# Kernel tuning notes

Hardware: AMD Instinct MI355X
Metric: run time of the kernel (lower is better)

The kernel has to match this reference:

```python
import jax, jax.numpy as jnp
import numpy as np

B = 524288   # samples
H = 16       # n_neuron[-1] for every node


def setup_inputs() -> dict:
    key = jax.random.key(0)
    ks = jax.random.split(key, 5)

    def w(k, shape, fan_in):
        return jax.random.normal(k, shape, jnp.float32) * (1.0 / np.sqrt(fan_in))

    return {
        "x":  jax.random.normal(ks[0], (B, 16), jnp.float32),
        # level 1: 8 nodes, each Linear(2 -> 16)
        "W1": w(ks[1], (8, 2, H), 2),  "b1": jnp.zeros((8, H), jnp.float32),
        # level 2: 4 nodes, each Linear(32 -> 16)
        "W2": w(ks[2], (4, 2 * H, H), 2 * H), "b2": jnp.zeros((4, H), jnp.float32),
        # level 3: 2 nodes, each Linear(32 -> 16)
        "W3": w(ks[3], (2, 2 * H, H), 2 * H), "b3": jnp.zeros((2, H), jnp.float32),
        # root: Linear(32 -> 16)
        "W4": w(ks[4], (2 * H, H), 2 * H),    "b4": jnp.zeros((H,), jnp.float32),
    }


def reference(x, W1, b1, W2, b2, W3, b3, W4, b4):
    b = x.shape[0]
    # Level 1: each node N1_i consumes leaves (L_{2i}, L_{2i+1}) -> concat == reshape
    h1 = jax.nn.relu(jnp.einsum('bnc,nch->bnh', x.reshape(b, 8, 2), W1) + b1)          # [B,8,16]
    # Level 2: node N2_i consumes concat(N1_{2i}, N1_{2i+1})
    h2 = jax.nn.relu(jnp.einsum('bnc,nch->bnh', h1.reshape(b, 4, 2 * H), W2) + b2)     # [B,4,16]
    # Level 3
    h3 = jax.nn.relu(jnp.einsum('bnc,nch->bnh', h2.reshape(b, 2, 2 * H), W3) + b3)     # [B,2,16]
    # Root N4_0
    out = jax.nn.relu(h3.reshape(b, 2 * H) @ W4 + b4)                                  # [B,16]
    return out
```

## Files before the change

kernel.cpp:

```cpp
#include <hip/hip_runtime.h>
#include <hip/hip_bf16.h>


typedef __attribute__((ext_vector_type(8))) short bf16x8;
typedef __attribute__((ext_vector_type(4))) float f32x4;

__device__ __forceinline__ short bfr(float f) {
  return (short)__builtin_bit_cast(unsigned short, __float2bfloat16(f));
}
__device__ __forceinline__ float relu_(float a) { return fmaxf(a, 0.0f); }

__global__ __launch_bounds__(256) void tree_mlp_mfma(
    const float* __restrict__ x,
    const float* __restrict__ W1, const float* __restrict__ b1,
    const float* __restrict__ W2, const float* __restrict__ b2,
    const float* __restrict__ W3, const float* __restrict__ b3,
    const float* __restrict__ W4, const float* __restrict__ b4,
    float* __restrict__ out, int ntiles) {
  const int lane = threadIdx.x & 63;
  const int n = lane & 15;
  const int g = lane >> 4;

  const int wpb = blockDim.x >> 6;
  const int gw = blockIdx.x * wpb + (threadIdx.x >> 6);
  const int nw = gridDim.x * wpb;

  bf16x8 w1f[8];
#pragma unroll
  for (int i = 0; i < 8; ++i) {
    bf16x8 f;
#pragma unroll
    for (int j = 0; j < 8; ++j) f[j] = (short)0;
#pragma unroll
    for (int j = 0; j < 4; ++j) {
      int k = 4 * g + j;
      float v = 0.0f;
      if (k == 2 * i)     v = W1[i * 32 + n];
      if (k == 2 * i + 1) v = W1[i * 32 + 16 + n];
      f[j] = bfr(v);
    }
    if (g == 0) f[4] = bfr(b1[i * 16 + n]);
    w1f[i] = f;
  }

  bf16x8 w2f[4]; f32x4 c2[4];
#pragma unroll
  for (int i = 0; i < 4; ++i) {
    bf16x8 f;
#pragma unroll
    for (int j = 0; j < 4; ++j) f[j]     = bfr(W2[i * 512 + (4 * g + j) * 16 + n]);
#pragma unroll
    for (int j = 0; j < 4; ++j) f[4 + j] = bfr(W2[i * 512 + (16 + 4 * g + j) * 16 + n]);
    w2f[i] = f;
#pragma unroll
    for (int r = 0; r < 4; ++r) c2[i][r] = b2[i * 16 + 4 * g + r];
  }
  bf16x8 w3f[2]; f32x4 c3[2];
#pragma unroll
  for (int i = 0; i < 2; ++i) {
    bf16x8 f;
#pragma unroll
    for (int j = 0; j < 4; ++j) f[j]     = bfr(W3[i * 512 + (4 * g + j) * 16 + n]);
#pragma unroll
    for (int j = 0; j < 4; ++j) f[4 + j] = bfr(W3[i * 512 + (16 + 4 * g + j) * 16 + n]);
    w3f[i] = f;
#pragma unroll
    for (int r = 0; r < 4; ++r) c3[i][r] = b3[i * 16 + 4 * g + r];
  }
  bf16x8 w4f; f32x4 c4;
  {
    bf16x8 f;
#pragma unroll
    for (int j = 0; j < 4; ++j) f[j]     = bfr(W4[(4 * g + j) * 16 + n]);
#pragma unroll
    for (int j = 0; j < 4; ++j) f[4 + j] = bfr(W4[(16 + 4 * g + j) * 16 + n]);
    w4f = f;
#pragma unroll
    for (int r = 0; r < 4; ++r) c4[r] = b4[4 * g + r];
  }

  const short one_bf = bfr(1.0f);
  const f32x4* __restrict__ xf = reinterpret_cast<const f32x4*>(x);
  f32x4* __restrict__ of = reinterpret_cast<f32x4*>(out);

  int t = gw;
  if (t >= ntiles) return;
  f32x4 xv = xf[(size_t)(t * 16 + n) * 4 + g];

  while (t < ntiles) {
    const int tn = t + nw;
    f32x4 xnext = xv;
    if (tn < ntiles) xnext = xf[(size_t)(tn * 16 + n) * 4 + g];

    bf16x8 xb;
    xb[0] = bfr(xv[0]); xb[1] = bfr(xv[1]); xb[2] = bfr(xv[2]); xb[3] = bfr(xv[3]);
    xb[4] = (g == 0) ? one_bf : (short)0;
    xb[5] = 0; xb[6] = 0; xb[7] = 0;

    const f32x4 zero = {0.f, 0.f, 0.f, 0.f};
    f32x4 a1[8];
#pragma unroll
    for (int i = 0; i < 8; ++i)
      a1[i] = __builtin_amdgcn_mfma_f32_16x16x32_bf16(w1f[i], xb, zero, 0, 0, 0);

    f32x4 a2[4];
#pragma unroll
    for (int i = 0; i < 4; ++i) {
      bf16x8 hb;
#pragma unroll
      for (int r = 0; r < 4; ++r) {
        hb[r]     = bfr(relu_(a1[2 * i][r]));
        hb[4 + r] = bfr(relu_(a1[2 * i + 1][r]));
      }
      a2[i] = __builtin_amdgcn_mfma_f32_16x16x32_bf16(w2f[i], hb, c2[i], 0, 0, 0);
    }

    f32x4 a3[2];
#pragma unroll
    for (int i = 0; i < 2; ++i) {
      bf16x8 hb;
#pragma unroll
      for (int r = 0; r < 4; ++r) {
        hb[r]     = bfr(relu_(a2[2 * i][r]));
        hb[4 + r] = bfr(relu_(a2[2 * i + 1][r]));
      }
      a3[i] = __builtin_amdgcn_mfma_f32_16x16x32_bf16(w3f[i], hb, c3[i], 0, 0, 0);
    }

    bf16x8 hb4;
#pragma unroll
    for (int r = 0; r < 4; ++r) {
      hb4[r]     = bfr(relu_(a3[0][r]));
      hb4[4 + r] = bfr(relu_(a3[1][r]));
    }
    f32x4 a4 = __builtin_amdgcn_mfma_f32_16x16x32_bf16(w4f, hb4, c4, 0, 0, 0);

    f32x4 o;
#pragma unroll
    for (int r = 0; r < 4; ++r) o[r] = relu_(a4[r]);
    __builtin_nontemporal_store(o, &of[(size_t)(t * 16 + n) * 4 + g]);

    t = tn;
    xv = xnext;
  }
}

extern "C" void kernel_launch(void* const* d_in, const int* in_sizes, int n_in,
                              void* d_out, int out_size, void* d_ws, size_t ws_size,
                              hipStream_t stream) {
  const float* x  = (const float*)d_in[0];
  const float* W1 = (const float*)d_in[1];
  const float* b1 = (const float*)d_in[2];
  const float* W2 = (const float*)d_in[3];
  const float* b2 = (const float*)d_in[4];
  const float* W3 = (const float*)d_in[5];
  const float* b3 = (const float*)d_in[6];
  const float* W4 = (const float*)d_in[7];
  const float* b4 = (const float*)d_in[8];
  float* out = (float*)d_out;

  const int ntiles = in_sizes[0] / 256;
  const int block = 256;
  const int grid = 1024;
  tree_mlp_mfma<<<grid, block, 0, stream>>>(x, W1, b1, W2, b2, W3, b3, W4, b4,
                                            out, ntiles);
}
```

Before: 29.90 us.

## Deepen input prefetch to two tiles, pack biases as bf16, tune occupancy

```diff
diff --git a/kernel.cpp b/kernel.cpp
--- a/kernel.cpp
+++ b/kernel.cpp
@@ -3,14 +3,25 @@
 
 
 typedef __attribute__((ext_vector_type(8))) short bf16x8;
+typedef __attribute__((ext_vector_type(4))) short bf16x4;
 typedef __attribute__((ext_vector_type(4))) float f32x4;
 
 __device__ __forceinline__ short bfr(float f) {
   return (short)__builtin_bit_cast(unsigned short, __float2bfloat16(f));
 }
+__device__ __forceinline__ float bf2f(short s) {
+  unsigned u = ((unsigned)(unsigned short)s) << 16;
+  return __builtin_bit_cast(float, u);
+}
 __device__ __forceinline__ float relu_(float a) { return fmaxf(a, 0.0f); }
+__device__ __forceinline__ f32x4 unpk(bf16x4 p) {
+  f32x4 c;
+#pragma unroll
+  for (int r = 0; r < 4; ++r) c[r] = bf2f(p[r]);
+  return c;
+}
 
-__global__ __launch_bounds__(256) void tree_mlp_mfma(
+__global__ __launch_bounds__(256, 3) void tree_mlp_mfma3(
     const float* __restrict__ x,
     const float* __restrict__ W1, const float* __restrict__ b1,
     const float* __restrict__ W2, const float* __restrict__ b2,
@@ -42,8 +53,7 @@
     if (g == 0) f[4] = bfr(b1[i * 16 + n]);
     w1f[i] = f;
   }
-
-  bf16x8 w2f[4]; f32x4 c2[4];
+  bf16x8 w2f[4]; bf16x4 c2p[4];
 #pragma unroll
   for (int i = 0; i < 4; ++i) {
     bf16x8 f;
@@ -53,9 +63,9 @@
     for (int j = 0; j < 4; ++j) f[4 + j] = bfr(W2[i * 512 + (16 + 4 * g + j) * 16 + n]);
     w2f[i] = f;
 #pragma unroll
-    for (int r = 0; r < 4; ++r) c2[i][r] = b2[i * 16 + 4 * g + r];
+    for (int r = 0; r < 4; ++r) c2p[i][r] = bfr(b2[i * 16 + 4 * g + r]);
   }
-  bf16x8 w3f[2]; f32x4 c3[2];
+  bf16x8 w3f[2]; bf16x4 c3p[2];
 #pragma unroll
   for (int i = 0; i < 2; ++i) {
     bf16x8 f;
@@ -65,9 +75,9 @@
     for (int j = 0; j < 4; ++j) f[4 + j] = bfr(W3[i * 512 + (16 + 4 * g + j) * 16 + n]);
     w3f[i] = f;
 #pragma unroll
-    for (int r = 0; r < 4; ++r) c3[i][r] = b3[i * 16 + 4 * g + r];
+    for (int r = 0; r < 4; ++r) c3p[i][r] = bfr(b3[i * 16 + 4 * g + r]);
   }
-  bf16x8 w4f; f32x4 c4;
+  bf16x8 w4f; bf16x4 c4p;
   {
     bf16x8 f;
 #pragma unroll
@@ -76,43 +86,45 @@
     for (int j = 0; j < 4; ++j) f[4 + j] = bfr(W4[(16 + 4 * g + j) * 16 + n]);
     w4f = f;
 #pragma unroll
-    for (int r = 0; r < 4; ++r) c4[r] = b4[4 * g + r];
+    for (int r = 0; r < 4; ++r) c4p[r] = bfr(b4[4 * g + r]);
   }
 
-  const short one_bf = bfr(1.0f);
+  const short bias_slot = (g == 0) ? bfr(1.0f) : (short)0;
   const f32x4* __restrict__ xf = reinterpret_cast<const f32x4*>(x);
   f32x4* __restrict__ of = reinterpret_cast<f32x4*>(out);
 
   int t = gw;
   if (t >= ntiles) return;
-  f32x4 xv = xf[(size_t)(t * 16 + n) * 4 + g];
 
-  while (t < ntiles) {
-    const int tn = t + nw;
-    f32x4 xnext = xv;
-    if (tn < ntiles) xnext = xf[(size_t)(tn * 16 + n) * 4 + g];
+  f32x4 xa = __builtin_nontemporal_load(&xf[(size_t)(t * 16 + n) * 4 + g]);
+  f32x4 xb1 = xa;
+  if (t + nw < ntiles)
+    xb1 = __builtin_nontemporal_load(&xf[(size_t)((t + nw) * 16 + n) * 4 + g]);
 
-    bf16x8 xb;
-    xb[0] = bfr(xv[0]); xb[1] = bfr(xv[1]); xb[2] = bfr(xv[2]); xb[3] = bfr(xv[3]);
-    xb[4] = (g == 0) ? one_bf : (short)0;
-    xb[5] = 0; xb[6] = 0; xb[7] = 0;
+  for (; t < ntiles; t += nw) {
+    f32x4 xc = xb1;
+    if (t + 2 * nw < ntiles)
+      xc = __builtin_nontemporal_load(&xf[(size_t)((t + 2 * nw) * 16 + n) * 4 + g]);
+
+    bf16x8 xbf;
+    xbf[0] = bfr(xa[0]); xbf[1] = bfr(xa[1]);
+    xbf[2] = bfr(xa[2]); xbf[3] = bfr(xa[3]);
+    xbf[4] = bias_slot; xbf[5] = 0; xbf[6] = 0; xbf[7] = 0;
 
     const f32x4 zero = {0.f, 0.f, 0.f, 0.f};
-    f32x4 a1[8];
-#pragma unroll
-    for (int i = 0; i < 8; ++i)
-      a1[i] = __builtin_amdgcn_mfma_f32_16x16x32_bf16(w1f[i], xb, zero, 0, 0, 0);
 
     f32x4 a2[4];
 #pragma unroll
     for (int i = 0; i < 4; ++i) {
+      f32x4 aL = __builtin_amdgcn_mfma_f32_16x16x32_bf16(w1f[2 * i],     xbf, zero, 0, 0, 0);
+      f32x4 aR = __builtin_amdgcn_mfma_f32_16x16x32_bf16(w1f[2 * i + 1], xbf, zero, 0, 0, 0);
       bf16x8 hb;
 #pragma unroll
       for (int r = 0; r < 4; ++r) {
-        hb[r]     = bfr(relu_(a1[2 * i][r]));
-        hb[4 + r] = bfr(relu_(a1[2 * i + 1][r]));
+        hb[r]     = bfr(relu_(aL[r]));
+        hb[4 + r] = bfr(relu_(aR[r]));
       }
-      a2[i] = __builtin_amdgcn_mfma_f32_16x16x32_bf16(w2f[i], hb, c2[i], 0, 0, 0);
+      a2[i] = __builtin_amdgcn_mfma_f32_16x16x32_bf16(w2f[i], hb, unpk(c2p[i]), 0, 0, 0);
     }
 
     f32x4 a3[2];
@@ -124,7 +136,7 @@
         hb[r]     = bfr(relu_(a2[2 * i][r]));
         hb[4 + r] = bfr(relu_(a2[2 * i + 1][r]));
       }
-      a3[i] = __builtin_amdgcn_mfma_f32_16x16x32_bf16(w3f[i], hb, c3[i], 0, 0, 0);
+      a3[i] = __builtin_amdgcn_mfma_f32_16x16x32_bf16(w3f[i], hb, unpk(c3p[i]), 0, 0, 0);
     }
 
     bf16x8 hb4;
@@ -133,15 +145,15 @@
       hb4[r]     = bfr(relu_(a3[0][r]));
       hb4[4 + r] = bfr(relu_(a3[1][r]));
     }
-    f32x4 a4 = __builtin_amdgcn_mfma_f32_16x16x32_bf16(w4f, hb4, c4, 0, 0, 0);
+    f32x4 a4 = __builtin_amdgcn_mfma_f32_16x16x32_bf16(w4f, hb4, unpk(c4p), 0, 0, 0);
 
     f32x4 o;
 #pragma unroll
     for (int r = 0; r < 4; ++r) o[r] = relu_(a4[r]);
     __builtin_nontemporal_store(o, &of[(size_t)(t * 16 + n) * 4 + g]);
 
-    t = tn;
-    xv = xnext;
+    xa = xb1;
+    xb1 = xc;
   }
 }
 
@@ -161,7 +173,7 @@
 
   const int ntiles = in_sizes[0] / 256;
   const int block = 256;
-  const int grid = 1024;
-  tree_mlp_mfma<<<grid, block, 0, stream>>>(x, W1, b1, W2, b2, W3, b3, W4, b4,
-                                            out, ntiles);
+  const int grid = 768;
+  tree_mlp_mfma3<<<grid, block, 0, stream>>>(x, W1, b1, W2, b2, W3, b3, W4, b4,
+                                             out, ntiles);
 }
```

After: 24.34 us. 1.23x faster.

## Process two tiles per wave iteration with interleaved MFMA chains

Applied to the files above, without the earlier changes.

```diff
diff --git a/kernel.cpp b/kernel.cpp
--- a/kernel.cpp
+++ b/kernel.cpp
@@ -10,7 +10,7 @@
 }
 __device__ __forceinline__ float relu_(float a) { return fmaxf(a, 0.0f); }
 
-__global__ __launch_bounds__(256) void tree_mlp_mfma(
+__global__ __launch_bounds__(256, 3) void tree_mlp_mfma4(
     const float* __restrict__ x,
     const float* __restrict__ W1, const float* __restrict__ b1,
     const float* __restrict__ W2, const float* __restrict__ b2,
@@ -42,7 +42,6 @@
     if (g == 0) f[4] = bfr(b1[i * 16 + n]);
     w1f[i] = f;
   }
-
   bf16x8 w2f[4]; f32x4 c2[4];
 #pragma unroll
   for (int i = 0; i < 4; ++i) {
@@ -79,69 +78,91 @@
     for (int r = 0; r < 4; ++r) c4[r] = b4[4 * g + r];
   }
 
-  const short one_bf = bfr(1.0f);
+  const short bias_slot = (g == 0) ? bfr(1.0f) : (short)0;
   const f32x4* __restrict__ xf = reinterpret_cast<const f32x4*>(x);
   f32x4* __restrict__ of = reinterpret_cast<f32x4*>(out);
 
-  int t = gw;
-  if (t >= ntiles) return;
-  f32x4 xv = xf[(size_t)(t * 16 + n) * 4 + g];
+  const int nsuper = ntiles >> 1;
+  int s = gw;
+  if (s >= nsuper) return;
 
-  while (t < ntiles) {
-    const int tn = t + nw;
-    f32x4 xnext = xv;
-    if (tn < ntiles) xnext = xf[(size_t)(tn * 16 + n) * 4 + g];
+  f32x4 xa0 = xf[(size_t)((2 * s)     * 16 + n) * 4 + g];
+  f32x4 xa1 = xf[(size_t)((2 * s + 1) * 16 + n) * 4 + g];
 
-    bf16x8 xb;
-    xb[0] = bfr(xv[0]); xb[1] = bfr(xv[1]); xb[2] = bfr(xv[2]); xb[3] = bfr(xv[3]);
-    xb[4] = (g == 0) ? one_bf : (short)0;
-    xb[5] = 0; xb[6] = 0; xb[7] = 0;
+  for (; s < nsuper; s += nw) {
+    const int sn = s + nw;
+    f32x4 xn0 = xa0, xn1 = xa1;
+    if (sn < nsuper) {
+      xn0 = xf[(size_t)((2 * sn)     * 16 + n) * 4 + g];
+      xn1 = xf[(size_t)((2 * sn + 1) * 16 + n) * 4 + g];
+    }
+
+    bf16x8 xb[2];
+#pragma unroll
+    for (int u = 0; u < 2; ++u) {
+      const f32x4 xv = (u == 0) ? xa0 : xa1;
+      bf16x8 f;
+      f[0] = bfr(xv[0]); f[1] = bfr(xv[1]); f[2] = bfr(xv[2]); f[3] = bfr(xv[3]);
+      f[4] = bias_slot; f[5] = 0; f[6] = 0; f[7] = 0;
+      xb[u] = f;
+    }
 
     const f32x4 zero = {0.f, 0.f, 0.f, 0.f};
-    f32x4 a1[8];
-#pragma unroll
-    for (int i = 0; i < 8; ++i)
-      a1[i] = __builtin_amdgcn_mfma_f32_16x16x32_bf16(w1f[i], xb, zero, 0, 0, 0);
 
-    f32x4 a2[4];
+    f32x4 a2[2][4];
 #pragma unroll
     for (int i = 0; i < 4; ++i) {
+#pragma unroll
+      for (int u = 0; u < 2; ++u) {
+        f32x4 aL = __builtin_amdgcn_mfma_f32_16x16x32_bf16(w1f[2 * i],     xb[u], zero, 0, 0, 0);
+        f32x4 aR = __builtin_amdgcn_mfma_f32_16x16x32_bf16(w1f[2 * i + 1], xb[u], zero, 0, 0, 0);
+        bf16x8 hb;
+#pragma unroll
+        for (int r = 0; r < 4; ++r) {
+          hb[r]     = bfr(relu_(aL[r]));
+          hb[4 + r] = bfr(relu_(aR[r]));
+        }
+        a2[u][i] = __builtin_amdgcn_mfma_f32_16x16x32_bf16(w2f[i], hb, c2[i], 0, 0, 0);
+      }
+    }
+
+    f32x4 a3[2][2];
+#pragma unroll
+    for (int i = 0; i < 2; ++i) {
+#pragma unroll
+      for (int u = 0; u < 2; ++u) {
+        bf16x8 hb;
+#pragma unroll
+        for (int r = 0; r < 4; ++r) {
+          hb[r]     = bfr(relu_(a2[u][2 * i][r]));
+          hb[4 + r] = bfr(relu_(a2[u][2 * i + 1][r]));
+        }
+        a3[u][i] = __builtin_amdgcn_mfma_f32_16x16x32_bf16(w3f[i], hb, c3[i], 0, 0, 0);
+      }
+    }
+
+    f32x4 a4[2];
+#pragma unroll
+    for (int u = 0; u < 2; ++u) {
       bf16x8 hb;
 #pragma unroll
       for (int r = 0; r < 4; ++r) {
-        hb[r]     = bfr(relu_(a1[2 * i][r]));
-        hb[4 + r] = bfr(relu_(a1[2 * i + 1][r]));
+        hb[r]     = bfr(relu_(a3[u][0][r]));
+        hb[4 + r] = bfr(relu_(a3[u][1][r]));
       }
-      a2[i] = __builtin_amdgcn_mfma_f32_16x16x32_bf16(w2f[i], hb, c2[i], 0, 0, 0);
+      a4[u] = __builtin_amdgcn_mfma_f32_16x16x32_bf16(w4f, hb, c4, 0, 0, 0);
     }
 
-    f32x4 a3[2];
 #pragma unroll
-    for (int i = 0; i < 2; ++i) {
-      bf16x8 hb;
+    for (int u = 0; u < 2; ++u) {
+      f32x4 o;
 #pragma unroll
-      for (int r = 0; r < 4; ++r) {
-        hb[r]     = bfr(relu_(a2[2 * i][r]));
-        hb[4 + r] = bfr(relu_(a2[2 * i + 1][r]));
-      }
-      a3[i] = __builtin_amdgcn_mfma_f32_16x16x32_bf16(w3f[i], hb, c3[i], 0, 0, 0);
+      for (int r = 0; r < 4; ++r) o[r] = relu_(a4[u][r]);
+      __builtin_nontemporal_store(o, &of[(size_t)((2 * s + u) * 16 + n) * 4 + g]);
     }
 
-    bf16x8 hb4;
-#pragma unroll
-    for (int r = 0; r < 4; ++r) {
-      hb4[r]     = bfr(relu_(a3[0][r]));
-      hb4[4 + r] = bfr(relu_(a3[1][r]));
-    }
-    f32x4 a4 = __builtin_amdgcn_mfma_f32_16x16x32_bf16(w4f, hb4, c4, 0, 0, 0);
-
-    f32x4 o;
-#pragma unroll
-    for (int r = 0; r < 4; ++r) o[r] = relu_(a4[r]);
-    __builtin_nontemporal_store(o, &of[(size_t)(t * 16 + n) * 4 + g]);
-
-    t = tn;
-    xv = xnext;
+    xa0 = xn0;
+    xa1 = xn1;
   }
 }
 
@@ -161,7 +182,7 @@
 
   const int ntiles = in_sizes[0] / 256;
   const int block = 256;
-  const int grid = 1024;
-  tree_mlp_mfma<<<grid, block, 0, stream>>>(x, W1, b1, W2, b2, W3, b3, W4, b4,
-                                            out, ntiles);
+  const int grid = 768;
+  tree_mlp_mfma4<<<grid, block, 0, stream>>>(x, W1, b1, W2, b2, W3, b3, W4, b4,
+                                             out, ntiles);
 }
```

New measurement: 24.58 us. -17.8%, faster.
